# Optimization experiments

Hardware: AMD Instinct MI355X
Metric: run time of the kernel (lower is better)

## Reference

```python
import jax, jax.numpy as jnp
import numpy as np

N_USER = 50000
N_ITEM = 50000
DIM = 128
HID = DIM // 2
E = 500000
SLOPE = 0.2  # GATv2 negative_slope default


def _glorot(key, shape):
    fan_in = shape[0]
    return jax.random.normal(key, shape, dtype=jnp.float32) / np.sqrt(fan_in)


def setup_inputs() -> dict:
    key = jax.random.key(0)
    ks = jax.random.split(key, 32)
    inp = {
        "x_user": jax.random.normal(ks[0], (N_USER, DIM), dtype=jnp.float32),
        "x_item": jax.random.normal(ks[1], (N_ITEM, DIM), dtype=jnp.float32),
        # edge[0] = source indices, edge[1] = destination indices
        "edge_u2i": jnp.stack([
            jax.random.randint(ks[2], (E,), 0, N_USER),
            jax.random.randint(ks[3], (E,), 0, N_ITEM),
        ]),
        "edge_i2u": jnp.stack([
            jax.random.randint(ks[4], (E,), 0, N_ITEM),
            jax.random.randint(ks[5], (E,), 0, N_USER),
        ]),
    }
    # per-node-type projection MLP: Linear(dim, dim//2) -> ReLU -> Linear(dim//2, dim)
    i = 6
    for t in ("user", "item"):
        inp[f"W1_{t}"] = _glorot(ks[i], (DIM, HID)); i += 1
        inp[f"b1_{t}"] = jnp.zeros((HID,), jnp.float32)
        inp[f"W2_{t}"] = _glorot(ks[i], (HID, DIM)); i += 1
        inp[f"b2_{t}"] = jnp.zeros((DIM,), jnp.float32)
    # per-edge-type GATv2 params (heads=1): lin_l (src), lin_r (dst), att, out bias
    for r in ("u2i", "i2u"):
        inp[f"Wl_{r}"] = _glorot(ks[i], (DIM, DIM)); i += 1
        inp[f"bl_{r}"] = jnp.zeros((DIM,), jnp.float32)
        inp[f"Wr_{r}"] = _glorot(ks[i], (DIM, DIM)); i += 1
        inp[f"br_{r}"] = jnp.zeros((DIM,), jnp.float32)
        inp[f"att_{r}"] = _glorot(ks[i], (DIM,)); i += 1
        inp[f"bias_{r}"] = jnp.zeros((DIM,), jnp.float32)
    return inp


def _mlp(x, W1, b1, W2, b2):
    return jax.nn.relu(x @ W1 + b1) @ W2 + b2


def _gatv2(x_src, x_dst, edge, Wl, bl, Wr, br, att, bias, n_dst):
    src, dst = edge[0], edge[1]
    xl = x_src @ Wl + bl                                    # [Ns, D]
    xr = x_dst @ Wr + br                                    # [Nd, D]
    z = jax.nn.leaky_relu(xl[src] + xr[dst], SLOPE)         # [E, D] gather
    logit = z @ att                                          # [E]
    # per-destination softmax over incoming edges
    m = jax.ops.segment_max(logit, dst, num_segments=n_dst)
    e = jnp.exp(logit - m[dst])
    s = jax.ops.segment_sum(e, dst, num_segments=n_dst)
    alpha = e / (s[dst] + 1e-16)                             # [E]
    out = jax.ops.segment_sum(alpha[:, None] * xl[src], dst, num_segments=n_dst)
    return out + bias


def reference(x_user, x_item, edge_u2i, edge_i2u,
              W1_user, b1_user, W2_user, b2_user,
              W1_item, b1_item, W2_item, b2_item,
              Wl_u2i, bl_u2i, Wr_u2i, br_u2i, att_u2i, bias_u2i,
              Wl_i2u, bl_i2u, Wr_i2u, br_i2u, att_i2u, bias_i2u):
    hu = _mlp(x_user, W1_user, b1_user, W2_user, b2_user)
    hi = _mlp(x_item, W1_item, b1_item, W2_item, b2_item)
    # HeteroConv with aggr='sum'; each dst type receives from one relation here
    out_item = _gatv2(hu, hi, edge_u2i, Wl_u2i, bl_u2i, Wr_u2i, br_u2i, att_u2i, bias_u2i, N_ITEM)
    out_user = _gatv2(hi, hu, edge_i2u, Wl_i2u, bl_i2u, Wr_i2u, br_i2u, att_i2u, bias_i2u, N_USER)
    return jnp.stack([out_user, out_item])  # [2, N, D] (N_USER == N_ITEM)
```

## Files before the change

kernel.cpp:

```cpp
#include <hip/hip_runtime.h>
#include <hip/hip_bf16.h>
#include <math.h>

#define N_NODES 50000
#define DIM 128
#define HID 64
#define SLOPE 0.2f
#define CAP 64

typedef __attribute__((ext_vector_type(8))) short bf16x8;
typedef __attribute__((ext_vector_type(4))) float f32x4;

#define OW1 0
#define OW2 8192
#define OWL 16384
#define OWR 32768
#define BLOB 49152
#define PREPB 192

static __device__ __forceinline__ ushort f2bf(float f) {
    uint u = __float_as_uint(f);
    u += 0x7FFFu + ((u >> 16) & 1u);
    return (ushort)(u >> 16);
}

static __device__ __forceinline__ void prep_one(
    const float* __restrict__ W1, const float* __restrict__ W2,
    const float* __restrict__ Wl, const float* __restrict__ Wr,
    ushort* __restrict__ blob, int idx)
{
    const float* W; int NN, nkt, rel;
    if (idx < OW2)      { W = W1; NN = 64;  nkt = 4; rel = idx; }
    else if (idx < OWL) { W = W2; NN = 128; nkt = 2; rel = idx - OW2; }
    else if (idx < OWR) { W = Wl; NN = 128; nkt = 4; rel = idx - OWL; }
    else                { W = Wr; NN = 128; nkt = 4; rel = idx - OWR; }
    int j = rel & 7, l = (rel >> 3) & 63, t = rel >> 9;
    int kt = t % nkt, n = t / nkt;
    int k   = kt * 32 + (l >> 4) * 8 + j;
    int col = n * 16 + (l & 15);
    blob[idx] = f2bf(W[k * NN + col]);
}

__global__ __launch_bounds__(256) void prep_weights(
    const float* __restrict__ W1u, const float* __restrict__ W2u,
    const float* __restrict__ Wlu, const float* __restrict__ Wru,
    ushort* __restrict__ blobU,
    const float* __restrict__ W1i, const float* __restrict__ W2i,
    const float* __restrict__ Wli, const float* __restrict__ Wri,
    ushort* __restrict__ blobI)
{
    int bid = blockIdx.x;
    const int idx = (bid % PREPB) * 256 + threadIdx.x;
    if (bid < PREPB) prep_one(W1u, W2u, Wlu, Wru, blobU, idx);
    else             prep_one(W1i, W2i, Wli, Wri, blobI, idx);
}

__global__ __launch_bounds__(512, 4) void k2_node_fill(
    const float* __restrict__ xA, const ushort* __restrict__ blobA,
    const float* __restrict__ b1A, const float* __restrict__ b2A,
    const float* __restrict__ blA, const float* __restrict__ brA,
    ushort* __restrict__ XLA, ushort* __restrict__ XRA,
    const float* __restrict__ xB, const ushort* __restrict__ blobB,
    const float* __restrict__ b1B, const float* __restrict__ b2B,
    const float* __restrict__ blB, const float* __restrict__ brB,
    ushort* __restrict__ XLB, ushort* __restrict__ XRB,
    int gnt, int M,
    const int* __restrict__ e1, int E1, const int* __restrict__ e2, int E2,
    int* __restrict__ counts2, int* __restrict__ slots, int fillCount)
{
    __shared__ ushort hstage_all[8 * 16 * 136];
    const int tid = threadIdx.x;

    int bid = blockIdx.x;
    int wid; bool isfill;
    const int twoF = fillCount * 2;
    if (bid < twoF) { isfill = (bid & 1); wid = bid >> 1; }
    else            { isfill = false;     wid = fillCount + (bid - twoF); }

    if (isfill) {
        const int t = wid * 512 + tid;
        const int n1 = (E1 + 7) >> 3;
        const int n2 = (E2 + 7) >> 3;
        const int *sp, *dp; int base, E, off;
        if (t < n1)           { sp = e1; dp = e1 + E1; base = t * 8;        E = E1; off = 0; }
        else if (t < n1 + n2) { sp = e2; dp = e2 + E2; base = (t - n1) * 8; E = E2; off = N_NODES; }
        else return;
        if (base + 8 <= E && ((E & 3) == 0)) {
            int4 s0 = *(const int4*)&sp[base];
            int4 s1 = *(const int4*)&sp[base + 4];
            int4 d0 = *(const int4*)&dp[base];
            int4 d1 = *(const int4*)&dp[base + 4];
            int di, pos;
            di = off + d0.x; pos = atomicAdd(&counts2[di], 1); if (pos < CAP) slots[di * CAP + pos] = s0.x;
            di = off + d0.y; pos = atomicAdd(&counts2[di], 1); if (pos < CAP) slots[di * CAP + pos] = s0.y;
            di = off + d0.z; pos = atomicAdd(&counts2[di], 1); if (pos < CAP) slots[di * CAP + pos] = s0.z;
            di = off + d0.w; pos = atomicAdd(&counts2[di], 1); if (pos < CAP) slots[di * CAP + pos] = s0.w;
            di = off + d1.x; pos = atomicAdd(&counts2[di], 1); if (pos < CAP) slots[di * CAP + pos] = s1.x;
            di = off + d1.y; pos = atomicAdd(&counts2[di], 1); if (pos < CAP) slots[di * CAP + pos] = s1.y;
            di = off + d1.z; pos = atomicAdd(&counts2[di], 1); if (pos < CAP) slots[di * CAP + pos] = s1.z;
            di = off + d1.w; pos = atomicAdd(&counts2[di], 1); if (pos < CAP) slots[di * CAP + pos] = s1.w;
        } else {
            int hi = min(E, base + 8);
            for (int k = base; k < hi; ++k) {
                int di = off + dp[k];
                int pos = atomicAdd(&counts2[di], 1);
                if (pos < CAP) slots[di * CAP + pos] = sp[k];
            }
        }
        return;
    }

    if (wid >= 2 * gnt) return;
    const float *x, *b1, *b2, *bl, *br;
    const ushort* blob;
    ushort *XL, *XR;
    int nbid = wid;
    if (nbid < gnt) {
        x = xA; blob = blobA; b1 = b1A; b2 = b2A; bl = blA; br = brA;
        XL = XLA; XR = XRA;
    } else {
        nbid -= gnt;
        x = xB; blob = blobB; b1 = b1B; b2 = b2B; bl = blB; br = brB;
        XL = XLB; XR = XRB;
    }

    const int wave = tid >> 6, lane = tid & 63;
    const int quad = lane & 15, half = lane >> 4;
    ushort* hstage = hstage_all + wave * (16 * 136);
    const int rbase = nbid * 256 + wave * 32;
    const int srow0 = min(rbase + quad,      M - 1);
    const int srow1 = min(rbase + 16 + quad, M - 1);

    bf16x8 a1[2][4];
    #pragma unroll
    for (int rt = 0; rt < 2; ++rt) {
        const int sr = rt ? srow1 : srow0;
        #pragma unroll
        for (int kt = 0; kt < 4; ++kt) {
            const float* p = &x[(size_t)sr * DIM + kt * 32 + half * 8];
            float4 f0 = *(const float4*)p;
            float4 f1 = *(const float4*)(p + 4);
            bf16x8 a;
            a[0] = (short)f2bf(f0.x); a[1] = (short)f2bf(f0.y);
            a[2] = (short)f2bf(f0.z); a[3] = (short)f2bf(f0.w);
            a[4] = (short)f2bf(f1.x); a[5] = (short)f2bf(f1.y);
            a[6] = (short)f2bf(f1.z); a[7] = (short)f2bf(f1.w);
            a1[rt][kt] = a;
        }
    }

    f32x4 hacc[2][4] = {};
    #pragma unroll
    for (int kt = 0; kt < 4; ++kt)
        #pragma unroll
        for (int n = 0; n < 4; ++n) {
            bf16x8 b = *(const bf16x8*)&blob[OW1 + (size_t)((n * 4 + kt) * 64 + lane) * 8];
            hacc[0][n] = __builtin_amdgcn_mfma_f32_16x16x32_bf16(b, a1[0][kt], hacc[0][n], 0, 0, 0);
            hacc[1][n] = __builtin_amdgcn_mfma_f32_16x16x32_bf16(b, a1[1][kt], hacc[1][n], 0, 0, 0);
        }

    bf16x8 a2[2][2];
    #pragma unroll
    for (int rt = 0; rt < 2; ++rt) {
        #pragma unroll
        for (int n = 0; n < 4; ++n) {
            const int col = n * 16 + half * 4;
            float4 bv = *(const float4*)&b1[col];
            ushort4 us;
            us.x = f2bf(fmaxf(hacc[rt][n][0] + bv.x, 0.f));
            us.y = f2bf(fmaxf(hacc[rt][n][1] + bv.y, 0.f));
            us.z = f2bf(fmaxf(hacc[rt][n][2] + bv.z, 0.f));
            us.w = f2bf(fmaxf(hacc[rt][n][3] + bv.w, 0.f));
            *(ushort4*)&hstage[quad * 136 + col] = us;
        }
        #pragma unroll
        for (int kt = 0; kt < 2; ++kt)
            a2[rt][kt] = *(const bf16x8*)&hstage[quad * 136 + kt * 32 + half * 8];
    }

    f32x4 h2acc[2][8] = {};
    #pragma unroll
    for (int kt = 0; kt < 2; ++kt)
        #pragma unroll
        for (int n = 0; n < 8; ++n) {
            bf16x8 b = *(const bf16x8*)&blob[OW2 + (size_t)((n * 2 + kt) * 64 + lane) * 8];
            h2acc[0][n] = __builtin_amdgcn_mfma_f32_16x16x32_bf16(b, a2[0][kt], h2acc[0][n], 0, 0, 0);
            h2acc[1][n] = __builtin_amdgcn_mfma_f32_16x16x32_bf16(b, a2[1][kt], h2acc[1][n], 0, 0, 0);
        }

    bf16x8 a3[2][4];
    #pragma unroll
    for (int rt = 0; rt < 2; ++rt) {
        #pragma unroll
        for (int n = 0; n < 8; ++n) {
            const int col = n * 16 + half * 4;
            float4 bv = *(const float4*)&b2[col];
            ushort4 us;
            us.x = f2bf(h2acc[rt][n][0] + bv.x);
            us.y = f2bf(h2acc[rt][n][1] + bv.y);
            us.z = f2bf(h2acc[rt][n][2] + bv.z);
            us.w = f2bf(h2acc[rt][n][3] + bv.w);
            *(ushort4*)&hstage[quad * 136 + col] = us;
        }
        #pragma unroll
        for (int kt = 0; kt < 4; ++kt)
            a3[rt][kt] = *(const bf16x8*)&hstage[quad * 136 + kt * 32 + half * 8];
    }

    const int r0 = rbase + quad;
    const int r1 = rbase + 16 + quad;
    #pragma unroll
    for (int n = 0; n < 8; ++n) {
        f32x4 aL0 = {}, aL1 = {}, aR0 = {}, aR1 = {};
        #pragma unroll
        for (int kt = 0; kt < 4; ++kt) {
            bf16x8 bL = *(const bf16x8*)&blob[OWL + (size_t)((n * 4 + kt) * 64 + lane) * 8];
            aL0 = __builtin_amdgcn_mfma_f32_16x16x32_bf16(bL, a3[0][kt], aL0, 0, 0, 0);
            aL1 = __builtin_amdgcn_mfma_f32_16x16x32_bf16(bL, a3[1][kt], aL1, 0, 0, 0);
            bf16x8 bR = *(const bf16x8*)&blob[OWR + (size_t)((n * 4 + kt) * 64 + lane) * 8];
            aR0 = __builtin_amdgcn_mfma_f32_16x16x32_bf16(bR, a3[0][kt], aR0, 0, 0, 0);
            aR1 = __builtin_amdgcn_mfma_f32_16x16x32_bf16(bR, a3[1][kt], aR1, 0, 0, 0);
        }
        const int col = n * 16 + half * 4;
        const float4 blv = *(const float4*)&bl[col];
        const float4 brv = *(const float4*)&br[col];
        if (r0 < M) {
            ushort4 ul, ur;
            ul.x = f2bf(aL0[0] + blv.x); ul.y = f2bf(aL0[1] + blv.y);
            ul.z = f2bf(aL0[2] + blv.z); ul.w = f2bf(aL0[3] + blv.w);
            ur.x = f2bf(aR0[0] + brv.x); ur.y = f2bf(aR0[1] + brv.y);
            ur.z = f2bf(aR0[2] + brv.z); ur.w = f2bf(aR0[3] + brv.w);
            *(ushort4*)&XL[(size_t)r0 * DIM + col] = ul;
            *(ushort4*)&XR[(size_t)r0 * DIM + col] = ur;
        }
        if (r1 < M) {
            ushort4 ul, ur;
            ul.x = f2bf(aL1[0] + blv.x); ul.y = f2bf(aL1[1] + blv.y);
            ul.z = f2bf(aL1[2] + blv.z); ul.w = f2bf(aL1[3] + blv.w);
            ur.x = f2bf(aR1[0] + brv.x); ur.y = f2bf(aR1[1] + brv.y);
            ur.z = f2bf(aR1[2] + brv.z); ur.w = f2bf(aR1[3] + brv.w);
            *(ushort4*)&XL[(size_t)r1 * DIM + col] = ul;
            *(ushort4*)&XR[(size_t)r1 * DIM + col] = ur;
        }
    }
}

static __device__ __forceinline__ void unpack_bf8(uint4 u, float* f) {
    f[0] = __uint_as_float(u.x << 16);
    f[1] = __uint_as_float(u.x & 0xFFFF0000u);
    f[2] = __uint_as_float(u.y << 16);
    f[3] = __uint_as_float(u.y & 0xFFFF0000u);
    f[4] = __uint_as_float(u.z << 16);
    f[5] = __uint_as_float(u.z & 0xFFFF0000u);
    f[6] = __uint_as_float(u.w << 16);
    f[7] = __uint_as_float(u.w & 0xFFFF0000u);
}

static __device__ __forceinline__ float edge_partial8(
    const float* a, const float* xr8, const float* at8)
{
    float p = 0.f;
    #pragma unroll
    for (int d = 0; d < 8; ++d) {
        float z = a[d] + xr8[d];
        z = fmaxf(z, SLOPE * z);
        p = fmaf(at8[d], z, p);
    }
    return p;
}

__global__ __launch_bounds__(256) void gat_both(
    const ushort* __restrict__ xlA, const ushort* __restrict__ xrA,
    const float* __restrict__ attA, const float* __restrict__ biasA,
    float* __restrict__ outA,
    const ushort* __restrict__ xlB, const ushort* __restrict__ xrB,
    const float* __restrict__ attB, const float* __restrict__ biasB,
    float* __restrict__ outB,
    const int* __restrict__ counts2, const int* __restrict__ slots)
{
    const int g    = (blockIdx.x * blockDim.x + threadIdx.x) >> 4;
    const int lane = threadIdx.x & 15;
    if (g >= 2 * N_NODES) return;

    const ushort *xl, *xr; const float *att, *bias; float* out; int gl;
    if (g < N_NODES) { xl = xlA; xr = xrA; att = attA; bias = biasA; out = outA; gl = g; }
    else { xl = xlB; xr = xrB; att = attB; bias = biasB; out = outB; gl = g - N_NODES; }

    float xr8[8], at8[8];
    unpack_bf8(*(const uint4*)&xr[(size_t)gl * DIM + lane * 8], xr8);
    *(float4*)&at8[0] = *(const float4*)&att[lane * 8];
    *(float4*)&at8[4] = *(const float4*)&att[lane * 8 + 4];

    const int start = g * CAP;
    int deg = counts2[g];
    if (deg > CAP) deg = CAP;

    float m = -INFINITY, s = 0.f;
    float acc[8] = {};

    int i = 0;
    for (; i + 2 <= deg; i += 2) {
        int s0 = slots[start + i];
        int s1 = slots[start + i + 1];
        float a0[8], a1[8];
        unpack_bf8(*(const uint4*)&xl[(size_t)s0 * DIM + lane * 8], a0);
        unpack_bf8(*(const uint4*)&xl[(size_t)s1 * DIM + lane * 8], a1);
        float p0 = edge_partial8(a0, xr8, at8);
        float p1 = edge_partial8(a1, xr8, at8);
        #pragma unroll
        for (int o = 8; o; o >>= 1) {
            p0 += __shfl_xor(p0, o, 16);
            p1 += __shfl_xor(p1, o, 16);
        }
        float mn = fmaxf(p0, p1);
        if (mn > m + 8.f) {
            float sc = __expf(m - mn);
            s *= sc;
            #pragma unroll
            for (int d = 0; d < 8; ++d) acc[d] *= sc;
            m = mn;
        }
        float w0 = __expf(p0 - m);
        float w1 = __expf(p1 - m);
        s += w0 + w1;
        #pragma unroll
        for (int d = 0; d < 8; ++d)
            acc[d] += w0 * a0[d] + w1 * a1[d];
    }
    if (i < deg) {
        int s0 = slots[start + i];
        float a0[8];
        unpack_bf8(*(const uint4*)&xl[(size_t)s0 * DIM + lane * 8], a0);
        float p0 = edge_partial8(a0, xr8, at8);
        #pragma unroll
        for (int o = 8; o; o >>= 1) p0 += __shfl_xor(p0, o, 16);
        if (p0 > m + 8.f) {
            float sc = __expf(m - p0);
            s *= sc;
            #pragma unroll
            for (int d = 0; d < 8; ++d) acc[d] *= sc;
            m = p0;
        }
        float w0 = __expf(p0 - m);
        s += w0;
        #pragma unroll
        for (int d = 0; d < 8; ++d) acc[d] += w0 * a0[d];
    }

    const float inv = 1.f / (s + 1e-16f);
    float o8[8];
    *(float4*)&o8[0] = *(const float4*)&bias[lane * 8];
    *(float4*)&o8[4] = *(const float4*)&bias[lane * 8 + 4];
    #pragma unroll
    for (int d = 0; d < 8; ++d) o8[d] = fmaf(acc[d], inv, o8[d]);
    float* op = &out[(size_t)gl * DIM + lane * 8];
    *(float4*)op       = *(const float4*)&o8[0];
    *(float4*)(op + 4) = *(const float4*)&o8[4];
}

extern "C" void kernel_launch(void* const* d_in, const int* in_sizes, int n_in,
                              void* d_out, int out_size, void* d_ws, size_t ws_size,
                              hipStream_t stream)
{
    const float* x_user   = (const float*)d_in[0];
    const float* x_item   = (const float*)d_in[1];
    const int*   edge_u2i = (const int*)d_in[2];
    const int*   edge_i2u = (const int*)d_in[3];
    const float* W1_user  = (const float*)d_in[4];
    const float* b1_user  = (const float*)d_in[5];
    const float* W2_user  = (const float*)d_in[6];
    const float* b2_user  = (const float*)d_in[7];
    const float* W1_item  = (const float*)d_in[8];
    const float* b1_item  = (const float*)d_in[9];
    const float* W2_item  = (const float*)d_in[10];
    const float* b2_item  = (const float*)d_in[11];
    const float* Wl_u2i   = (const float*)d_in[12];
    const float* bl_u2i   = (const float*)d_in[13];
    const float* Wr_u2i   = (const float*)d_in[14];
    const float* br_u2i   = (const float*)d_in[15];
    const float* att_u2i  = (const float*)d_in[16];
    const float* bias_u2i = (const float*)d_in[17];
    const float* Wl_i2u   = (const float*)d_in[18];
    const float* bl_i2u   = (const float*)d_in[19];
    const float* Wr_i2u   = (const float*)d_in[20];
    const float* br_i2u   = (const float*)d_in[21];
    const float* att_i2u  = (const float*)d_in[22];
    const float* bias_i2u = (const float*)d_in[23];

    const int E1 = in_sizes[2] / 2;
    const int E2 = in_sizes[3] / 2;

    const size_t NF = (size_t)N_NODES * DIM;
    ushort* XLu = (ushort*)d_ws;
    ushort* XRu = XLu + NF;
    ushort* XLi = XRu + NF;
    ushort* XRi = XLi + NF;
    ushort* blobU = XRi + NF;
    ushort* blobI = blobU + BLOB;
    int* counts2 = (int*)(blobI + BLOB);
    int* slots   = counts2 + 2 * N_NODES;

    float* out_user = (float*)d_out;
    float* out_item = out_user + NF;

    dim3 blk(256);

    hipMemsetAsync(counts2, 0, 2 * N_NODES * sizeof(int), stream);

    prep_weights<<<2 * PREPB, blk, 0, stream>>>(
        W1_user, W2_user, Wl_u2i, Wr_i2u, blobU,
        W1_item, W2_item, Wl_i2u, Wr_u2i, blobI);

    const int nthr8 = ((E1 + 7) / 8) + ((E2 + 7) / 8);
    const int gnt = (N_NODES + 255) / 256;
    const int nodeCount = 2 * gnt;
    const int fillCount = (nthr8 + 511) / 512;
    const int totalB = nodeCount + fillCount;
    k2_node_fill<<<totalB, dim3(512), 0, stream>>>(
        x_user, blobU, b1_user, b2_user, bl_u2i, br_i2u, XLu, XRu,
        x_item, blobI, b1_item, b2_item, bl_i2u, br_u2i, XLi, XRi,
        gnt, N_NODES,
        edge_u2i, E1, edge_i2u, E2, counts2, slots, fillCount);

    const int ng = (2 * N_NODES * 16 + 255) / 256;
    gat_both<<<ng, blk, 0, stream>>>(XLu, XRi, att_u2i, bias_u2i, out_item,
                                     XLi, XRu, att_i2u, bias_i2u, out_user,
                                     counts2, slots);
}
```

Before: 146.1 us.

## Store neighbor slots as 16-bit, fold count reset into prep, raise MFMA priority

Changes the per-destination neighbor slot table from int32 to uint16, since node indices stay below 65536. This halves slot-table scatter and read traffic. The separate memset of the degree counters moves into the weight-prep kernel, which saves one launch. s_setprio is also raised around the MFMA loops in the node kernel. The 16-bit slots would break if the node count ever exceeded 65535.

```diff
diff --git a/kernel.cpp b/kernel.cpp
--- a/kernel.cpp
+++ b/kernel.cpp
@@ -47,12 +47,17 @@
     ushort* __restrict__ blobU,
     const float* __restrict__ W1i, const float* __restrict__ W2i,
     const float* __restrict__ Wli, const float* __restrict__ Wri,
-    ushort* __restrict__ blobI)
-{
-    int bid = blockIdx.x;
-    const int idx = (bid % PREPB) * 256 + threadIdx.x;
-    if (bid < PREPB) prep_one(W1u, W2u, Wlu, Wru, blobU, idx);
-    else             prep_one(W1i, W2i, Wli, Wri, blobI, idx);
+    ushort* __restrict__ blobI,
+    int* __restrict__ counts2)
+{
+    const int bid = blockIdx.x;
+    const int gtid = bid * 256 + threadIdx.x;
+    if (gtid < 2 * N_NODES) counts2[gtid] = 0;
+    if (bid < PREPB) {
+        prep_one(W1u, W2u, Wlu, Wru, blobU, bid * 256 + threadIdx.x);
+    } else if (bid < 2 * PREPB) {
+        prep_one(W1i, W2i, Wli, Wri, blobI, (bid - PREPB) * 256 + threadIdx.x);
+    }
 }
 
 __global__ __launch_bounds__(512, 4) void k2_node_fill(
@@ -66,7 +71,7 @@
     ushort* __restrict__ XLB, ushort* __restrict__ XRB,
     int gnt, int M,
     const int* __restrict__ e1, int E1, const int* __restrict__ e2, int E2,
-    int* __restrict__ counts2, int* __restrict__ slots, int fillCount)
+    int* __restrict__ counts2, ushort* __restrict__ slots16, int fillCount)
 {
     __shared__ ushort hstage_all[8 * 16 * 136];
     const int tid = threadIdx.x;
@@ -91,20 +96,20 @@
             int4 d0 = *(const int4*)&dp[base];
             int4 d1 = *(const int4*)&dp[base + 4];
             int di, pos;
-            di = off + d0.x; pos = atomicAdd(&counts2[di], 1); if (pos < CAP) slots[di * CAP + pos] = s0.x;
-            di = off + d0.y; pos = atomicAdd(&counts2[di], 1); if (pos < CAP) slots[di * CAP + pos] = s0.y;
-            di = off + d0.z; pos = atomicAdd(&counts2[di], 1); if (pos < CAP) slots[di * CAP + pos] = s0.z;
-            di = off + d0.w; pos = atomicAdd(&counts2[di], 1); if (pos < CAP) slots[di * CAP + pos] = s0.w;
-            di = off + d1.x; pos = atomicAdd(&counts2[di], 1); if (pos < CAP) slots[di * CAP + pos] = s1.x;
-            di = off + d1.y; pos = atomicAdd(&counts2[di], 1); if (pos < CAP) slots[di * CAP + pos] = s1.y;
-            di = off + d1.z; pos = atomicAdd(&counts2[di], 1); if (pos < CAP) slots[di * CAP + pos] = s1.z;
-            di = off + d1.w; pos = atomicAdd(&counts2[di], 1); if (pos < CAP) slots[di * CAP + pos] = s1.w;
+            di = off + d0.x; pos = atomicAdd(&counts2[di], 1); if (pos < CAP) slots16[di * CAP + pos] = (ushort)s0.x;
+            di = off + d0.y; pos = atomicAdd(&counts2[di], 1); if (pos < CAP) slots16[di * CAP + pos] = (ushort)s0.y;
+            di = off + d0.z; pos = atomicAdd(&counts2[di], 1); if (pos < CAP) slots16[di * CAP + pos] = (ushort)s0.z;
+            di = off + d0.w; pos = atomicAdd(&counts2[di], 1); if (pos < CAP) slots16[di * CAP + pos] = (ushort)s0.w;
+            di = off + d1.x; pos = atomicAdd(&counts2[di], 1); if (pos < CAP) slots16[di * CAP + pos] = (ushort)s1.x;
+            di = off + d1.y; pos = atomicAdd(&counts2[di], 1); if (pos < CAP) slots16[di * CAP + pos] = (ushort)s1.y;
+            di = off + d1.z; pos = atomicAdd(&counts2[di], 1); if (pos < CAP) slots16[di * CAP + pos] = (ushort)s1.z;
+            di = off + d1.w; pos = atomicAdd(&counts2[di], 1); if (pos < CAP) slots16[di * CAP + pos] = (ushort)s1.w;
         } else {
             int hi = min(E, base + 8);
             for (int k = base; k < hi; ++k) {
                 int di = off + dp[k];
                 int pos = atomicAdd(&counts2[di], 1);
-                if (pos < CAP) slots[di * CAP + pos] = sp[k];
+                if (pos < CAP) slots16[di * CAP + pos] = (ushort)sp[k];
             }
         }
         return;
@@ -150,6 +155,7 @@
     }
 
     f32x4 hacc[2][4] = {};
+    __builtin_amdgcn_s_setprio(1);
     #pragma unroll
     for (int kt = 0; kt < 4; ++kt)
         #pragma unroll
@@ -158,6 +164,7 @@
             hacc[0][n] = __builtin_amdgcn_mfma_f32_16x16x32_bf16(b, a1[0][kt], hacc[0][n], 0, 0, 0);
             hacc[1][n] = __builtin_amdgcn_mfma_f32_16x16x32_bf16(b, a1[1][kt], hacc[1][n], 0, 0, 0);
         }
+    __builtin_amdgcn_s_setprio(0);
 
     bf16x8 a2[2][2];
     #pragma unroll
@@ -179,6 +186,7 @@
     }
 
     f32x4 h2acc[2][8] = {};
+    __builtin_amdgcn_s_setprio(1);
     #pragma unroll
     for (int kt = 0; kt < 2; ++kt)
         #pragma unroll
@@ -187,6 +195,7 @@
             h2acc[0][n] = __builtin_amdgcn_mfma_f32_16x16x32_bf16(b, a2[0][kt], h2acc[0][n], 0, 0, 0);
             h2acc[1][n] = __builtin_amdgcn_mfma_f32_16x16x32_bf16(b, a2[1][kt], h2acc[1][n], 0, 0, 0);
         }
+    __builtin_amdgcn_s_setprio(0);
 
     bf16x8 a3[2][4];
     #pragma unroll
@@ -212,6 +221,7 @@
     #pragma unroll
     for (int n = 0; n < 8; ++n) {
         f32x4 aL0 = {}, aL1 = {}, aR0 = {}, aR1 = {};
+        __builtin_amdgcn_s_setprio(1);
         #pragma unroll
         for (int kt = 0; kt < 4; ++kt) {
             bf16x8 bL = *(const bf16x8*)&blob[OWL + (size_t)((n * 4 + kt) * 64 + lane) * 8];
@@ -221,6 +231,7 @@
             aR0 = __builtin_amdgcn_mfma_f32_16x16x32_bf16(bR, a3[0][kt], aR0, 0, 0, 0);
             aR1 = __builtin_amdgcn_mfma_f32_16x16x32_bf16(bR, a3[1][kt], aR1, 0, 0, 0);
         }
+        __builtin_amdgcn_s_setprio(0);
         const int col = n * 16 + half * 4;
         const float4 blv = *(const float4*)&bl[col];
         const float4 brv = *(const float4*)&br[col];
@@ -276,7 +287,7 @@
     const ushort* __restrict__ xlB, const ushort* __restrict__ xrB,
     const float* __restrict__ attB, const float* __restrict__ biasB,
     float* __restrict__ outB,
-    const int* __restrict__ counts2, const int* __restrict__ slots)
+    const int* __restrict__ counts2, const ushort* __restrict__ slots16)
 {
     const int g    = (blockIdx.x * blockDim.x + threadIdx.x) >> 4;
     const int lane = threadIdx.x & 15;
@@ -300,8 +311,8 @@
 
     int i = 0;
     for (; i + 2 <= deg; i += 2) {
-        int s0 = slots[start + i];
-        int s1 = slots[start + i + 1];
+        int s0 = slots16[start + i];
+        int s1 = slots16[start + i + 1];
         float a0[8], a1[8];
         unpack_bf8(*(const uint4*)&xl[(size_t)s0 * DIM + lane * 8], a0);
         unpack_bf8(*(const uint4*)&xl[(size_t)s1 * DIM + lane * 8], a1);
@@ -328,7 +339,7 @@
             acc[d] += w0 * a0[d] + w1 * a1[d];
     }
     if (i < deg) {
-        int s0 = slots[start + i];
+        int s0 = slots16[start + i];
         float a0[8];
         unpack_bf8(*(const uint4*)&xl[(size_t)s0 * DIM + lane * 8], a0);
         float p0 = edge_partial8(a0, xr8, at8);
@@ -397,19 +408,19 @@
     ushort* XRi = XLi + NF;
     ushort* blobU = XRi + NF;
     ushort* blobI = blobU + BLOB;
-    int* counts2 = (int*)(blobI + BLOB);
-    int* slots   = counts2 + 2 * N_NODES;
+    int*    counts2 = (int*)(blobI + BLOB);
+    ushort* slots16 = (ushort*)(counts2 + 2 * N_NODES);
 
     float* out_user = (float*)d_out;
     float* out_item = out_user + NF;
 
     dim3 blk(256);
 
-    hipMemsetAsync(counts2, 0, 2 * N_NODES * sizeof(int), stream);
-
-    prep_weights<<<2 * PREPB, blk, 0, stream>>>(
+    const int prepGrid = (2 * N_NODES + 255) / 256;
+    prep_weights<<<(prepGrid > 2 * PREPB ? prepGrid : 2 * PREPB), blk, 0, stream>>>(
         W1_user, W2_user, Wl_u2i, Wr_i2u, blobU,
-        W1_item, W2_item, Wl_i2u, Wr_u2i, blobI);
+        W1_item, W2_item, Wl_i2u, Wr_u2i, blobI,
+        counts2);
 
     const int nthr8 = ((E1 + 7) / 8) + ((E2 + 7) / 8);
     const int gnt = (N_NODES + 255) / 256;
@@ -420,10 +431,10 @@
         x_user, blobU, b1_user, b2_user, bl_u2i, br_i2u, XLu, XRu,
         x_item, blobI, b1_item, b2_item, bl_i2u, br_u2i, XLi, XRi,
         gnt, N_NODES,
-        edge_u2i, E1, edge_i2u, E2, counts2, slots, fillCount);
+        edge_u2i, E1, edge_i2u, E2, counts2, slots16, fillCount);
 
     const int ng = (2 * N_NODES * 16 + 255) / 256;
     gat_both<<<ng, blk, 0, stream>>>(XLu, XRi, att_u2i, bias_u2i, out_item,
                                      XLi, XRu, att_i2u, bias_i2u, out_user,
-                                     counts2, slots);
-}
+                                     counts2, slots16);
+}
```

Result: slower. 149.5 us (+2.3%).
